# Performance work log

Measured on AMD Instinct MI355X. Metric: run time of the kernel, lower is better.

## Reference

```python
import jax, jax.numpy as jnp
import numpy as np

EPS = 1e-12  # torch F.normalize eps


def _unfold(x, k, pad, stride):
    # torch F.unfold: [B,C,H,W] -> [B, C*k*k, L], channel-major then kernel (i,j)
    B, C, H, W = x.shape
    xp = jnp.pad(x, ((0, 0), (0, 0), (pad, pad), (pad, pad)))
    Ho = (H + 2 * pad - k) // stride + 1
    Wo = (W + 2 * pad - k) // stride + 1
    patches = [xp[:, :, i:i + stride * (Ho - 1) + 1:stride, j:j + stride * (Wo - 1) + 1:stride]
               for i in range(k) for j in range(k)]
    p = jnp.stack(patches, axis=2)  # [B, C, k*k, Ho, Wo]
    return p.reshape(B, C * k * k, Ho * Wo)


def _fold(t, out_hw, k, pad, stride):
    # torch F.fold: [B, C*k*k, L] -> [B, C, H, W] with overlap-add
    B, Ckk, L = t.shape
    C = Ckk // (k * k)
    H, W = out_hw
    Ho = (H + 2 * pad - k) // stride + 1
    Wo = (W + 2 * pad - k) // stride + 1
    t = t.reshape(B, C, k, k, Ho, Wo)
    out = jnp.zeros((B, C, H + 2 * pad, W + 2 * pad), t.dtype)
    for i in range(k):
        for j in range(k):
            out = out.at[:, :, i:i + stride * (Ho - 1) + 1:stride,
                         j:j + stride * (Wo - 1) + 1:stride].add(t[:, :, i, j])
    return out[:, :, pad:pad + H, pad:pad + W]


def setup_inputs() -> dict:
    key = jax.random.key(0)
    ks = jax.random.split(key, 5)
    B, C3, H3 = 4, 256, 48
    return {
        'dh_img_lv3': jax.random.normal(ks[0], (B, C3, H3, H3), jnp.float32),
        'dh_ref_lv3': jax.random.normal(ks[1], (B, C3, H3, H3), jnp.float32),
        'cl_ref_lv1': jax.random.normal(ks[2], (B, 64, H3 * 4, H3 * 4), jnp.float32),
        'cl_ref_lv2': jax.random.normal(ks[3], (B, 128, H3 * 2, H3 * 2), jnp.float32),
        'cl_ref_lv3': jax.random.normal(ks[4], (B, C3, H3, H3), jnp.float32),
    }


def reference(dh_img_lv3, dh_ref_lv3, cl_ref_lv1, cl_ref_lv2, cl_ref_lv3):
    ksz, pad = 3, 1
    B, C3, H3, W3 = dh_img_lv3.shape

    q = _unfold(dh_img_lv3, ksz, pad, 1)                      # [B, D, Lq]
    kmat = _unfold(dh_ref_lv3, ksz, pad, 1).transpose(0, 2, 1)  # [B, Lk, D]
    kmat = kmat / jnp.maximum(jnp.linalg.norm(kmat, axis=2, keepdims=True), EPS)
    q = q / jnp.maximum(jnp.linalg.norm(q, axis=1, keepdims=True), EPS)

    rel = jnp.einsum('bld,bdm->blm', kmat, q)                 # [B, Lk, Lq]
    rel_val = jnp.max(rel, axis=1, keepdims=True)             # [B, 1, Lq]  (top-1, k=1)
    rel_idx = jnp.argmax(rel, axis=1, keepdims=True)          # [B, 1, Lq]

    v3 = _unfold(cl_ref_lv3, ksz, pad, 1)                     # [B, C3*9,   Lk]
    v2 = _unfold(cl_ref_lv2, 2 * ksz, 2 * pad, 2)             # [B, C2*36,  Lk]
    v1 = _unfold(cl_ref_lv1, 4 * ksz, 4 * pad, 4)             # [B, C1*144, Lk]

    def transfer(v):
        idx = jnp.broadcast_to(rel_idx, (B, v.shape[1], rel_idx.shape[2]))
        tv = jnp.take_along_axis(v, idx, axis=2)              # [B, Cv, Lq]
        # weighted sum over k=1 topk / sum of weights (faithful to original)
        return (rel_val * tv) / rel_val

    T3u, T2u, T1u = transfer(v3), transfer(v2), transfer(v1)

    def fold_norm(Tu, scale, k_, p_, s_):
        hw = (H3 * scale, W3 * scale)
        cnt = _fold(jnp.ones_like(Tu), hw, k_, p_, s_)
        return _fold(Tu, hw, k_, p_, s_) / cnt

    T_lv3 = fold_norm(T3u, 1, ksz, pad, 1)
    T_lv2 = fold_norm(T2u, 2, 2 * ksz, 2 * pad, 2)
    T_lv1 = fold_norm(T1u, 4, 4 * ksz, 4 * pad, 4)

    S = rel_val.reshape(B, 1, H3, W3)
    return S, T_lv3, T_lv2, T_lv1
```

## Files before the change

### kernel.cpp

```cpp
#include <hip/hip_runtime.h>


__global__ __launch_bounds__(256) void k_pixsq(const float* __restrict__ img,
                                               const float* __restrict__ ref,
                                               float* __restrict__ psi,
                                               float* __restrict__ psr) {
  int pix = blockIdx.x * 256 + threadIdx.x;
  int b = pix / 2304, p = pix - b * 2304;
  const float* ib = img + (size_t)b * 256 * 2304 + p;
  const float* rb = ref + (size_t)b * 256 * 2304 + p;
  float si = 0.f, sr = 0.f;
#pragma unroll 8
  for (int c = 0; c < 256; ++c) {
    float x = ib[c * 2304]; si = fmaf(x, x, si);
    float y = rb[c * 2304]; sr = fmaf(y, y, sr);
  }
  psi[pix] = si; psr[pix] = sr;
}

__global__ __launch_bounds__(256) void k_norm(const float* __restrict__ psr,
                                              const float* __restrict__ psi,
                                              float* __restrict__ kn,
                                              float* __restrict__ qn) {
  int pix = blockIdx.x * 256 + threadIdx.x;
  int b = pix / 2304, p = pix - b * 2304;
  int py = p / 48, px = p - py * 48;
  float sr = 0.f, si = 0.f;
#pragma unroll
  for (int dy = -1; dy <= 1; ++dy) {
#pragma unroll
    for (int dx = -1; dx <= 1; ++dx) {
      if (py + dy < 0 || py + dy >= 48 || px + dx < 0 || px + dx >= 48) continue;
      int n = pix + dy * 48 + dx;
      sr += psr[n]; si += psi[n];
    }
  }
  kn[pix] = fmaxf(sqrtf(sr), 1e-12f);
  qn[pix] = fmaxf(sqrtf(si), 1e-12f);
}

__global__ __launch_bounds__(256) void k_gemm(const float* __restrict__ A,
                                              const float* __restrict__ Bm,
                                              float* __restrict__ S) {
  __shared__ float As[8][128];
  __shared__ float Bs[8][128];
  const int t = threadIdx.x;
  const int q0 = blockIdx.y * 128, p0 = blockIdx.x * 128;
  const int lr = t >> 5, lc = (t & 31) << 2;
  const int tq = t >> 4, tp = t & 15;
  float acc[8][8];
#pragma unroll
  for (int u = 0; u < 8; ++u)
#pragma unroll
    for (int v = 0; v < 8; ++v) acc[u][v] = 0.f;

  for (int c0 = 0; c0 < 256; c0 += 8) {
    float4 a4 = *(const float4*)(A  + (c0 + lr) * 2304 + q0 + lc);
    float4 b4 = *(const float4*)(Bm + (c0 + lr) * 2304 + p0 + lc);
    __syncthreads();
    *(float4*)(&As[lr][lc]) = a4;
    *(float4*)(&Bs[lr][lc]) = b4;
    __syncthreads();
#pragma unroll
    for (int kk = 0; kk < 8; ++kk) {
      float4 a0 = *(const float4*)(&As[kk][tq * 8]);
      float4 a1 = *(const float4*)(&As[kk][tq * 8 + 4]);
      float4 b0 = *(const float4*)(&Bs[kk][tp * 4]);
      float4 b1 = *(const float4*)(&Bs[kk][64 + tp * 4]);
      float av[8] = {a0.x, a0.y, a0.z, a0.w, a1.x, a1.y, a1.z, a1.w};
      float bv[8] = {b0.x, b0.y, b0.z, b0.w, b1.x, b1.y, b1.z, b1.w};
#pragma unroll
      for (int u = 0; u < 8; ++u)
#pragma unroll
        for (int v = 0; v < 8; ++v)
          acc[u][v] = fmaf(av[u], bv[v], acc[u][v]);
    }
  }
#pragma unroll
  for (int u = 0; u < 8; ++u) {
    int q = q0 + tq * 8 + u;
    float* o = S + (size_t)q * 2304 + p0;
    *(float4*)(o + tp * 4)      = make_float4(acc[u][0], acc[u][1], acc[u][2], acc[u][3]);
    *(float4*)(o + 64 + tp * 4) = make_float4(acc[u][4], acc[u][5], acc[u][6], acc[u][7]);
  }
}

__global__ __launch_bounds__(256) void k_argmax(const float* __restrict__ S,
                                                const float* __restrict__ kn,
                                                const float* __restrict__ qn,
                                                int* __restrict__ oidx,
                                                float* __restrict__ oval) {
  const int q = blockIdx.x;
  const int qy = q / 48, qx = q - qy * 48;
  const int t = threadIdx.x;
  float best = -1e30f; int bidx = 0;
  for (int k = 0; k < 9; ++k) {
    int p = (k << 8) + t;
    int py = p / 48, px = p - py * 48;
    float s = 0.f;
#pragma unroll
    for (int dy = -1; dy <= 1; ++dy) {
      if (qy + dy < 0 || qy + dy >= 48) continue;
#pragma unroll
      for (int dx = -1; dx <= 1; ++dx) {
        if (qx + dx < 0 || qx + dx >= 48) continue;
        if (py + dy >= 0 && py + dy < 48 && px + dx >= 0 && px + dx < 48)
          s += S[(size_t)(q + dy * 48 + dx) * 2304 + (p + dy * 48 + dx)];
      }
    }
    float v = s / kn[p];
    if (v > best || (v == best && p < bidx)) { best = v; bidx = p; }
  }
  int lane = t & 63, wid = t >> 6;
#pragma unroll
  for (int off = 32; off; off >>= 1) {
    float ov = __shfl_down(best, off);
    int   oi = __shfl_down(bidx, off);
    if (ov > best || (ov == best && oi < bidx)) { best = ov; bidx = oi; }
  }
  __shared__ float sv[4];
  __shared__ int   si4[4];
  if (lane == 0) { sv[wid] = best; si4[wid] = bidx; }
  __syncthreads();
  if (t == 0) {
#pragma unroll
    for (int i = 1; i < 4; ++i)
      if (sv[i] > best || (sv[i] == best && si4[i] < bidx)) { best = sv[i]; bidx = si4[i]; }
    oidx[q] = bidx;
    oval[q] = best / qn[q];
  }
}

__global__ __launch_bounds__(256) void k_fold(const float* __restrict__ cl,
                                              const int* __restrict__ ridx,
                                              float* __restrict__ out,
                                              int Cc, int sc, int Hh) {
  int tid = blockIdx.x * 256 + threadIdx.x;
  int w = tid % Hh;
  int r1 = tid / Hh;
  int h = r1 % Hh;
  int r2 = r1 / Hh;
  int c = r2 % Cc;
  int b = r2 / Cc;
  int hi = h / sc, hr = h - hi * sc;
  int wi = w / sc, wr = w - wi * sc;
  float sum = 0.f; int cnt = 0;
  for (int ii = 0; ii < 3; ++ii) {
    int oy = hi + 1 - ii;
    if (oy < 0 || oy >= 48) continue;
    for (int jj = 0; jj < 3; ++jj) {
      int ox = wi + 1 - jj;
      if (ox < 0 || ox >= 48) continue;
      ++cnt;
      int m = ridx[b * 2304 + oy * 48 + ox];
      int my = m / 48, mx = m - my * 48;
      int y = sc * (my - 1 + ii) + hr;
      int x = sc * (mx - 1 + jj) + wr;
      if (y >= 0 && y < Hh && x >= 0 && x < Hh)
        sum += cl[(((size_t)b * Cc + c) * Hh + y) * Hh + x];
    }
  }
  out[tid] = sum / (float)cnt;
}

extern "C" void kernel_launch(void* const* d_in, const int* in_sizes, int n_in,
                              void* d_out, int out_size, void* d_ws, size_t ws_size,
                              hipStream_t stream) {
  const float* img = (const float*)d_in[0];
  const float* ref = (const float*)d_in[1];
  const float* cl1 = (const float*)d_in[2];
  const float* cl2 = (const float*)d_in[3];
  const float* cl3 = (const float*)d_in[4];
  float* out = (float*)d_out;

  float* ws   = (float*)d_ws;
  float* ps_i = ws;
  float* ps_r = ws + 9216;
  float* kn   = ws + 18432;
  float* qn   = ws + 27648;
  int*   ridx = (int*)(ws + 36864);
  float* S    = ws + 46080;

  k_pixsq<<<36, 256, 0, stream>>>(img, ref, ps_i, ps_r);
  k_norm<<<36, 256, 0, stream>>>(ps_r, ps_i, kn, qn);

  for (int b = 0; b < 4; ++b) {
    k_gemm<<<dim3(18, 18), 256, 0, stream>>>(img + b * 589824, ref + b * 589824, S);
    k_argmax<<<2304, 256, 0, stream>>>(S, kn + b * 2304, qn + b * 2304,
                                       ridx + b * 2304, out + b * 2304);
  }

  k_fold<<<9216, 256, 0, stream>>>(cl3, ridx, out + 9216,    256, 1, 48);
  k_fold<<<18432, 256, 0, stream>>>(cl2, ridx, out + 2368512, 128, 2, 96);
  k_fold<<<36864, 256, 0, stream>>>(cl1, ridx, out + 7087104, 64, 4, 192);
}
```

Before: 811.0 us.

## Batch GEMM/argmax over z, tile argmax in LDS, transpose-then-gather fold

Several changes land together. The channel-norm kernel now splits channels across threads and reduces through shared memory, and norms are stored as reciprocals. GEMM and argmax are batched over the batch dimension when the workspace allows. The argmax handles a 2x2 query block per CTA from an LDS tile of S rows, replacing scattered per-query global reads. The fold is rebuilt as a channel-last transpose followed by a gather with coalesced channel reads, all meant to cut uncoalesced memory traffic and launch count, at the cost of extra transpose passes and a larger workspace.

```diff
diff --git a/kernel.cpp b/kernel.cpp
--- a/kernel.cpp
+++ b/kernel.cpp
@@ -1,29 +1,44 @@
 #include <hip/hip_runtime.h>
 
+
+#define HW3 2304
+#define PLANE 589824
+#define SSTRIDE 5308416LL
 
 __global__ __launch_bounds__(256) void k_pixsq(const float* __restrict__ img,
                                                const float* __restrict__ ref,
                                                float* __restrict__ psi,
                                                float* __restrict__ psr) {
-  int pix = blockIdx.x * 256 + threadIdx.x;
-  int b = pix / 2304, p = pix - b * 2304;
-  const float* ib = img + (size_t)b * 256 * 2304 + p;
-  const float* rb = ref + (size_t)b * 256 * 2304 + p;
+  __shared__ float ri[16][17], rr[16][17];
+  int t = threadIdx.x;
+  int pl = t & 15, cg = t >> 4;
+  int pix = blockIdx.x * 16 + pl;
+  int b = pix / HW3, p = pix - b * HW3;
+  const float* ib = img + (size_t)b * PLANE + p;
+  const float* rb = ref + (size_t)b * PLANE + p;
   float si = 0.f, sr = 0.f;
-#pragma unroll 8
-  for (int c = 0; c < 256; ++c) {
-    float x = ib[c * 2304]; si = fmaf(x, x, si);
-    float y = rb[c * 2304]; sr = fmaf(y, y, sr);
-  }
-  psi[pix] = si; psr[pix] = sr;
+#pragma unroll
+  for (int c = 0; c < 16; ++c) {
+    float x = ib[(cg * 16 + c) * HW3]; si = fmaf(x, x, si);
+    float y = rb[(cg * 16 + c) * HW3]; sr = fmaf(y, y, sr);
+  }
+  ri[pl][cg] = si; rr[pl][cg] = sr;
+  __syncthreads();
+  if (t < 16) {
+    float a = 0.f, s2 = 0.f;
+#pragma unroll
+    for (int g = 0; g < 16; ++g) { a += ri[t][g]; s2 += rr[t][g]; }
+    int pix2 = blockIdx.x * 16 + t;
+    psi[pix2] = a; psr[pix2] = s2;
+  }
 }
 
 __global__ __launch_bounds__(256) void k_norm(const float* __restrict__ psr,
                                               const float* __restrict__ psi,
-                                              float* __restrict__ kn,
-                                              float* __restrict__ qn) {
+                                              float* __restrict__ ikn,
+                                              float* __restrict__ iqn) {
   int pix = blockIdx.x * 256 + threadIdx.x;
-  int b = pix / 2304, p = pix - b * 2304;
+  int b = pix / HW3, p = pix - b * HW3;
   int py = p / 48, px = p - py * 48;
   float sr = 0.f, si = 0.f;
 #pragma unroll
@@ -35,15 +50,19 @@
       sr += psr[n]; si += psi[n];
     }
   }
-  kn[pix] = fmaxf(sqrtf(sr), 1e-12f);
-  qn[pix] = fmaxf(sqrtf(si), 1e-12f);
-}
-
-__global__ __launch_bounds__(256) void k_gemm(const float* __restrict__ A,
-                                              const float* __restrict__ Bm,
-                                              float* __restrict__ S) {
+  ikn[pix] = 1.0f / fmaxf(sqrtf(sr), 1e-12f);
+  iqn[pix] = 1.0f / fmaxf(sqrtf(si), 1e-12f);
+}
+
+__global__ __launch_bounds__(256) void k_gemm(const float* __restrict__ img,
+                                              const float* __restrict__ ref,
+                                              float* __restrict__ S,
+                                              int b0, long long sstride) {
   __shared__ float As[8][128];
   __shared__ float Bs[8][128];
+  const float* A  = img + (size_t)(b0 + blockIdx.z) * PLANE;
+  const float* Bm = ref + (size_t)(b0 + blockIdx.z) * PLANE;
+  float* Sb = S + (size_t)blockIdx.z * sstride;
   const int t = threadIdx.x;
   const int q0 = blockIdx.y * 128, p0 = blockIdx.x * 128;
   const int lr = t >> 5, lc = (t & 31) << 2;
@@ -55,8 +74,8 @@
     for (int v = 0; v < 8; ++v) acc[u][v] = 0.f;
 
   for (int c0 = 0; c0 < 256; c0 += 8) {
-    float4 a4 = *(const float4*)(A  + (c0 + lr) * 2304 + q0 + lc);
-    float4 b4 = *(const float4*)(Bm + (c0 + lr) * 2304 + p0 + lc);
+    float4 a4 = *(const float4*)(A  + (c0 + lr) * HW3 + q0 + lc);
+    float4 b4 = *(const float4*)(Bm + (c0 + lr) * HW3 + p0 + lc);
     __syncthreads();
     *(float4*)(&As[lr][lc]) = a4;
     *(float4*)(&Bs[lr][lc]) = b4;
@@ -79,93 +98,185 @@
 #pragma unroll
   for (int u = 0; u < 8; ++u) {
     int q = q0 + tq * 8 + u;
-    float* o = S + (size_t)q * 2304 + p0;
+    float* o = Sb + (size_t)q * HW3 + p0;
     *(float4*)(o + tp * 4)      = make_float4(acc[u][0], acc[u][1], acc[u][2], acc[u][3]);
     *(float4*)(o + 64 + tp * 4) = make_float4(acc[u][4], acc[u][5], acc[u][6], acc[u][7]);
   }
 }
 
-__global__ __launch_bounds__(256) void k_argmax(const float* __restrict__ S,
-                                                const float* __restrict__ kn,
-                                                const float* __restrict__ qn,
-                                                int* __restrict__ oidx,
-                                                float* __restrict__ oval) {
-  const int q = blockIdx.x;
-  const int qy = q / 48, qx = q - qy * 48;
+__global__ __launch_bounds__(256) void k_argmax2(const float* __restrict__ S,
+                                                 const float* __restrict__ ikn,
+                                                 const float* __restrict__ iqn,
+                                                 int* __restrict__ oidx,
+                                                 float* __restrict__ oval,
+                                                 int b0, long long sstride) {
+  __shared__ float L[16][354];
+  __shared__ float rv[4][4];
+  __shared__ int   ri4[4][4];
+  const int b = b0 + blockIdx.z;
+  const float* Sb = S + (size_t)blockIdx.z * sstride;
+  const float* iknb = ikn + b * HW3;
+  const float* iqnb = iqn + b * HW3;
+  const int qy0 = blockIdx.y * 2, qx0 = blockIdx.x * 2;
   const int t = threadIdx.x;
-  float best = -1e30f; int bidx = 0;
-  for (int k = 0; k < 9; ++k) {
-    int p = (k << 8) + t;
-    int py = p / 48, px = p - py * 48;
-    float s = 0.f;
-#pragma unroll
-    for (int dy = -1; dy <= 1; ++dy) {
-      if (qy + dy < 0 || qy + dy >= 48) continue;
-#pragma unroll
-      for (int dx = -1; dx <= 1; ++dx) {
-        if (qx + dx < 0 || qx + dx >= 48) continue;
-        if (py + dy >= 0 && py + dy < 48 && px + dx >= 0 && px + dx < 48)
-          s += S[(size_t)(q + dy * 48 + dx) * 2304 + (p + dy * 48 + dx)];
+
+  float best[4]; int bid[4];
+#pragma unroll
+  for (int i = 0; i < 4; ++i) { best[i] = -1e30f; bid[i] = 0; }
+
+  for (int pc = 0; pc < 9; ++pc) {
+    const int cbase = pc * 256 - 49;
+    for (int e = t; e < 16 * 354; e += 256) {
+      int row = e / 354, col = e - row * 354;
+      int u = row >> 2, v = row & 3;
+      int ry = qy0 - 1 + u, rx = qx0 - 1 + v;
+      int c = cbase + col;
+      float val = 0.f;
+      if (ry >= 0 && ry < 48 && rx >= 0 && rx < 48 && c >= 0 && c < HW3)
+        val = Sb[(size_t)(ry * 48 + rx) * HW3 + c];
+      L[row][col] = val;
+    }
+    __syncthreads();
+    const int p = pc * 256 + t;
+    const int py = p / 48, px = p - py * 48;
+#pragma unroll
+    for (int a = 0; a < 2; ++a)
+#pragma unroll
+      for (int bb = 0; bb < 2; ++bb) {
+        const int qy = qy0 + a, qx = qx0 + bb;
+        float s = 0.f;
+#pragma unroll
+        for (int dy = -1; dy <= 1; ++dy) {
+          if (qy + dy < 0 || qy + dy >= 48 || py + dy < 0 || py + dy >= 48) continue;
+#pragma unroll
+          for (int dx = -1; dx <= 1; ++dx) {
+            if (qx + dx < 0 || qx + dx >= 48 || px + dx < 0 || px + dx >= 48) continue;
+            s += L[(a + dy + 1) * 4 + (bb + dx + 1)][t + 49 + dy * 48 + dx];
+          }
+        }
+        float v = s * iknb[p];
+        int qi = a * 2 + bb;
+        if (v > best[qi]) { best[qi] = v; bid[qi] = p; }
       }
-    }
-    float v = s / kn[p];
-    if (v > best || (v == best && p < bidx)) { best = v; bidx = p; }
-  }
-  int lane = t & 63, wid = t >> 6;
-#pragma unroll
-  for (int off = 32; off; off >>= 1) {
-    float ov = __shfl_down(best, off);
-    int   oi = __shfl_down(bidx, off);
-    if (ov > best || (ov == best && oi < bidx)) { best = ov; bidx = oi; }
-  }
-  __shared__ float sv[4];
-  __shared__ int   si4[4];
-  if (lane == 0) { sv[wid] = best; si4[wid] = bidx; }
+    __syncthreads();
+  }
+
+  int lane = t & 63, wv = t >> 6;
+#pragma unroll
+  for (int qi = 0; qi < 4; ++qi) {
+    float bv = best[qi]; int bi = bid[qi];
+#pragma unroll
+    for (int off = 32; off; off >>= 1) {
+      float ov = __shfl_down(bv, off);
+      int   oi = __shfl_down(bi, off);
+      if (ov > bv || (ov == bv && oi < bi)) { bv = ov; bi = oi; }
+    }
+    if (lane == 0) { rv[qi][wv] = bv; ri4[qi][wv] = bi; }
+  }
   __syncthreads();
-  if (t == 0) {
-#pragma unroll
-    for (int i = 1; i < 4; ++i)
-      if (sv[i] > best || (sv[i] == best && si4[i] < bidx)) { best = sv[i]; bidx = si4[i]; }
-    oidx[q] = bidx;
-    oval[q] = best / qn[q];
-  }
-}
-
-__global__ __launch_bounds__(256) void k_fold(const float* __restrict__ cl,
-                                              const int* __restrict__ ridx,
-                                              float* __restrict__ out,
-                                              int Cc, int sc, int Hh) {
-  int tid = blockIdx.x * 256 + threadIdx.x;
-  int w = tid % Hh;
-  int r1 = tid / Hh;
-  int h = r1 % Hh;
-  int r2 = r1 / Hh;
-  int c = r2 % Cc;
-  int b = r2 / Cc;
-  int hi = h / sc, hr = h - hi * sc;
-  int wi = w / sc, wr = w - wi * sc;
-  float sum = 0.f; int cnt = 0;
-  for (int ii = 0; ii < 3; ++ii) {
-    int oy = hi + 1 - ii;
-    if (oy < 0 || oy >= 48) continue;
-    for (int jj = 0; jj < 3; ++jj) {
-      int ox = wi + 1 - jj;
-      if (ox < 0 || ox >= 48) continue;
-      ++cnt;
-      int m = ridx[b * 2304 + oy * 48 + ox];
+  if (t < 4) {
+    float bv = rv[t][0]; int bi = ri4[t][0];
+#pragma unroll
+    for (int w = 1; w < 4; ++w)
+      if (rv[t][w] > bv || (rv[t][w] == bv && ri4[t][w] < bi)) { bv = rv[t][w]; bi = ri4[t][w]; }
+    int qy = qy0 + (t >> 1), qx = qx0 + (t & 1), q = qy * 48 + qx;
+    oidx[b * HW3 + q] = bi;
+    oval[b * HW3 + q] = bv * iqnb[q];
+  }
+}
+
+__global__ __launch_bounds__(256) void k_tr(const float* __restrict__ src,
+                                            float* __restrict__ dst,
+                                            int C, int HW, int b0) {
+  __shared__ float sm[64][65];
+  int pix0 = blockIdx.x * 64, c0 = blockIdx.y * 64;
+  const float* s = src + (size_t)(b0 + blockIdx.z) * C * HW;
+  float* d = dst + (size_t)blockIdx.z * HW * C;
+  int lane = threadIdx.x & 63, q4 = threadIdx.x >> 6;
+#pragma unroll
+  for (int r = 0; r < 16; ++r) {
+    int cl = r * 4 + q4;
+    sm[cl][lane] = s[(size_t)(c0 + cl) * HW + pix0 + lane];
+  }
+  __syncthreads();
+#pragma unroll
+  for (int r = 0; r < 16; ++r) {
+    int pl = r * 4 + q4;
+    d[(size_t)(pix0 + pl) * C + c0 + lane] = sm[lane][pl];
+  }
+}
+
+__global__ __launch_bounds__(256) void k_foldgather(const float* __restrict__ t,
+                                                    const int* __restrict__ ridx,
+                                                    float* __restrict__ out,
+                                                    int C, int H, int sc, int b0) {
+  __shared__ int   soff[64][9];
+  __shared__ float sicnt[64];
+  __shared__ float tr[64][65];
+  const int HW = H * H;
+  const int b = b0 + blockIdx.y;
+  const float* tb = t + (size_t)blockIdx.y * HW * C;
+  const int* rb = ridx + b * HW3;
+  const int pix0 = blockIdx.x * 64;
+
+  for (int e = threadIdx.x; e < 576; e += 256) {
+    int op = e / 9, tap = e - op * 9;
+    int pix = pix0 + op;
+    int h = pix / H, w = pix - h * H;
+    int hi = h / sc, hr = h - hi * sc;
+    int wi = w / sc, wr = w - wi * sc;
+    int ii = tap / 3, jj = tap - ii * 3;
+    int oy = hi + 1 - ii, ox = wi + 1 - jj;
+    int off = -1;
+    if (oy >= 0 && oy < 48 && ox >= 0 && ox < 48) {
+      int m = rb[oy * 48 + ox];
       int my = m / 48, mx = m - my * 48;
       int y = sc * (my - 1 + ii) + hr;
       int x = sc * (mx - 1 + jj) + wr;
-      if (y >= 0 && y < Hh && x >= 0 && x < Hh)
-        sum += cl[(((size_t)b * Cc + c) * Hh + y) * Hh + x];
-    }
-  }
-  out[tid] = sum / (float)cnt;
+      if (y >= 0 && y < H && x >= 0 && x < H) off = y * H + x;
+    }
+    soff[op][tap] = off;
+    if (tap == 0) {
+      int cnt = 0;
+#pragma unroll
+      for (int i2 = 0; i2 < 3; ++i2)
+#pragma unroll
+        for (int j2 = 0; j2 < 3; ++j2) {
+          int oy2 = hi + 1 - i2, ox2 = wi + 1 - j2;
+          if (oy2 >= 0 && oy2 < 48 && ox2 >= 0 && ox2 < 48) ++cnt;
+        }
+      sicnt[op] = 1.0f / (float)cnt;
+    }
+  }
+  __syncthreads();
+
+  const int g = threadIdx.x >> 6, lane = threadIdx.x & 63;
+  for (int c0 = 0; c0 < C; c0 += 64) {
+#pragma unroll
+    for (int o = 0; o < 16; ++o) {
+      int op = g * 16 + o;
+      float s = 0.f;
+#pragma unroll
+      for (int tp = 0; tp < 9; ++tp) {
+        int off = soff[op][tp];
+        if (off >= 0) s += tb[(size_t)off * C + c0 + lane];
+      }
+      tr[op][lane] = s * sicnt[op];
+    }
+    __syncthreads();
+#pragma unroll
+    for (int r = 0; r < 16; ++r) {
+      int cl = r * 4 + g;
+      out[((size_t)b * C + c0 + cl) * HW + pix0 + lane] = tr[lane][cl];
+    }
+    __syncthreads();
+  }
 }
 
 extern "C" void kernel_launch(void* const* d_in, const int* in_sizes, int n_in,
                               void* d_out, int out_size, void* d_ws, size_t ws_size,
                               hipStream_t stream) {
+  (void)in_sizes; (void)n_in; (void)out_size;
   const float* img = (const float*)d_in[0];
   const float* ref = (const float*)d_in[1];
   const float* cl1 = (const float*)d_in[2];
@@ -176,21 +287,41 @@
   float* ws   = (float*)d_ws;
   float* ps_i = ws;
   float* ps_r = ws + 9216;
-  float* kn   = ws + 18432;
-  float* qn   = ws + 27648;
+  float* ikn  = ws + 18432;
+  float* iqn  = ws + 27648;
   int*   ridx = (int*)(ws + 36864);
   float* S    = ws + 46080;
 
-  k_pixsq<<<36, 256, 0, stream>>>(img, ref, ps_i, ps_r);
-  k_norm<<<36, 256, 0, stream>>>(ps_r, ps_i, kn, qn);
-
-  for (int b = 0; b < 4; ++b) {
-    k_gemm<<<dim3(18, 18), 256, 0, stream>>>(img + b * 589824, ref + b * 589824, S);
-    k_argmax<<<2304, 256, 0, stream>>>(S, kn + b * 2304, qn + b * 2304,
-                                       ridx + b * 2304, out + b * 2304);
-  }
-
-  k_fold<<<9216, 256, 0, stream>>>(cl3, ridx, out + 9216,    256, 1, 48);
-  k_fold<<<18432, 256, 0, stream>>>(cl2, ridx, out + 2368512, 128, 2, 96);
-  k_fold<<<36864, 256, 0, stream>>>(cl1, ridx, out + 7087104, 64, 4, 192);
-}
+  const long long availf = (long long)(ws_size / 4) - 46080;
+  const bool bigS   = availf >= 4 * SSTRIDE;
+  const bool lv1all = availf >= 9437184LL;
+
+  k_pixsq<<<576, 256, 0, stream>>>(img, ref, ps_i, ps_r);
+  k_norm<<<36, 256, 0, stream>>>(ps_r, ps_i, ikn, iqn);
+
+  if (bigS) {
+    k_gemm<<<dim3(18, 18, 4), 256, 0, stream>>>(img, ref, S, 0, SSTRIDE);
+    k_argmax2<<<dim3(24, 24, 4), 256, 0, stream>>>(S, ikn, iqn, ridx, out, 0, SSTRIDE);
+  } else {
+    for (int b = 0; b < 4; ++b) {
+      k_gemm<<<dim3(18, 18, 1), 256, 0, stream>>>(img, ref, S, b, 0LL);
+      k_argmax2<<<dim3(24, 24, 1), 256, 0, stream>>>(S, ikn, iqn, ridx, out, b, 0LL);
+    }
+  }
+
+  float* t = S;
+
+  k_tr<<<dim3(36, 4, 4), 256, 0, stream>>>(cl3, t, 256, 2304, 0);
+  k_foldgather<<<dim3(36, 4), 256, 0, stream>>>(t, ridx, out + 9216, 256, 48, 1, 0);
+  k_tr<<<dim3(144, 2, 4), 256, 0, stream>>>(cl2, t, 128, 9216, 0);
+  k_foldgather<<<dim3(144, 4), 256, 0, stream>>>(t, ridx, out + 2368512, 128, 96, 2, 0);
+  if (lv1all) {
+    k_tr<<<dim3(576, 1, 4), 256, 0, stream>>>(cl1, t, 64, 36864, 0);
+    k_foldgather<<<dim3(576, 4), 256, 0, stream>>>(t, ridx, out + 7087104, 64, 192, 4, 0);
+  } else {
+    for (int b = 0; b < 4; ++b) {
+      k_tr<<<dim3(576, 1, 1), 256, 0, stream>>>(cl1, t, 64, 36864, b);
+      k_foldgather<<<dim3(576, 1), 256, 0, stream>>>(t, ridx, out + 7087104, 64, 192, 4, b);
+    }
+  }
+}
```

After: 807.3 us. About the same (-0.5%).
